# Optimization experiments

Measured on AMD Instinct MI355X. Metric: run time of the kernel, lower is better.

The kernel has to match this reference:

```python
import jax, jax.numpy as jnp
import numpy as np

B, N, F_IN, H = 16, 1024, 64, 256
NEG = -9e15
ALPHA = 0.2  # LeakyReLU slope


def _leaky(x):
    return jnp.where(x >= 0, x, ALPHA * x)


def setup_inputs() -> dict:
    key = jax.random.key(0)
    ks = jax.random.split(key, 12)
    s = lambda k, shape, fan: jax.random.normal(k, shape, jnp.float32) / np.sqrt(fan)
    node_features = jax.random.normal(ks[0], (B, N, F_IN), jnp.float32)
    adj_matrix = jax.random.randint(ks[1], (B, N, N), 0, 2).astype(jnp.float32)
    return {
        "node_features": node_features,
        "adj_matrix": adj_matrix,
        "emb_W": s(ks[2], (F_IN, H), F_IN),
        "emb_b": jnp.zeros((H,), jnp.float32),
        "W0": s(ks[3], (H, H), H),
        "a1_0": s(ks[4], (H,), H),
        "a2_0": s(ks[5], (H,), H),
        "W1": s(ks[6], (H, H), H),
        "a1_1": s(ks[7], (H,), H),
        "a2_1": s(ks[8], (H,), H),
        "gp_W1": s(ks[9], (H, H), H),
        "gp_b1": jnp.zeros((H,), jnp.float32),
        "gp_W2": s(ks[10], (H, H), H),
        "gp_b2": jnp.zeros((H,), jnp.float32),
    }


def _gat_layer(x, mask, W, a1, a2):
    # x: [B,N,H]; mask: [B,N,N] bool. Equivalent to original concat trick:
    # a([h_i || h_j]) = h_i @ a1 + h_j @ a2 with a.weight split in halves.
    h = jnp.einsum('bnf,fo->bno', x, W)              # [B,N,H]
    s1 = jnp.einsum('bnh,h->bn', h, a1)              # [B,N]
    s2 = jnp.einsum('bnh,h->bn', h, a2)              # [B,N]
    e = _leaky(s1[:, :, None] + s2[:, None, :])      # [B,N,N]
    att = jax.nn.softmax(jnp.where(mask, e, NEG), axis=2)
    # dropout p=0.2 is identity in eval mode
    return jnp.einsum('bij,bjh->bih', att, h)        # [B,N,H]


def reference(node_features, adj_matrix, emb_W, emb_b,
              W0, a1_0, a2_0, W1, a1_1, a2_1,
              gp_W1, gp_b1, gp_W2, gp_b2):
    mask = adj_matrix > 0
    x = jnp.einsum('bnf,fh->bnh', node_features, emb_W) + emb_b
    x = jax.nn.relu(_gat_layer(x, mask, W0, a1_0, a2_0))
    x = jax.nn.relu(_gat_layer(x, mask, W1, a1_1, a2_1))
    g = jnp.mean(x, axis=1) + jnp.max(x, axis=1)     # [B,H]
    g = jax.nn.relu(g @ gp_W1 + gp_b1) @ gp_W2 + gp_b2
    return x, g
```

## Files before the change

kernel.cpp:

```cpp
#include <hip/hip_runtime.h>
#include <hip/hip_bf16.h>

#define B 16
#define N 1024
#define F_IN 64
#define H 256
#define ALPHA 0.2f

typedef __attribute__((ext_vector_type(8))) _Float16 half8;
typedef __attribute__((ext_vector_type(4))) _Float16 half4;
typedef __attribute__((ext_vector_type(4))) float floatx4;

__device__ __forceinline__ floatx4 mfma_f16(half8 a, half8 b, floatx4 c) {
    return __builtin_amdgcn_mfma_f32_16x16x32_f16(a, b, c, 0, 0, 0);
}

__global__ __launch_bounds__(256) void k_front(const float* __restrict__ adj,
                                               const float* __restrict__ nf,
                                               const float* __restrict__ embW,
                                               const float* __restrict__ embB,
                                               const float* __restrict__ W0, const float* __restrict__ W1,
                                               const float* __restrict__ a10, const float* __restrict__ a20,
                                               const float* __restrict__ a11, const float* __restrict__ a21,
                                               unsigned* __restrict__ mask32,
                                               _Float16* __restrict__ xf,
                                               _Float16* __restrict__ wBf,
                                               float* __restrict__ wa1, float* __restrict__ wa2) {
    __shared__ float lds[256 * 17];
    const int blk = blockIdx.x;
    const int t = threadIdx.x;
    const int lane = t & 63;

    if (blk < 1024) {
        const int wv = blk * 4 + (t >> 6);
#pragma unroll 2
        for (int task = wv; task < B * N * 4; task += 4096) {
            const float4 v = *(const float4*)(adj + (size_t)task * 256 + lane * 4);
            unsigned long long b0 = __ballot(v.x > 0.f);
            unsigned long long b1 = __ballot(v.y > 0.f);
            unsigned long long b2 = __ballot(v.z > 0.f);
            unsigned long long b3 = __ballot(v.w > 0.f);
            if (lane < 8) {
                unsigned w0 = (unsigned)((b0 >> (8 * lane)) & 0xff)
                            | ((unsigned)((b1 >> (8 * lane)) & 0xff) << 8)
                            | ((unsigned)((b2 >> (8 * lane)) & 0xff) << 16)
                            | ((unsigned)((b3 >> (8 * lane)) & 0xff) << 24);
                const int jg = task & 3, row = task >> 2;
                mask32[(size_t)row * 32 + jg * 8 + lane] = w0;
            }
        }
        return;
    }
    if (blk < 1536) {
        const int row0 = (blk - 1024) * 32;
        float* nfs = lds;
        for (int idx = t; idx < 32 * F_IN; idx += 256) {
            int r = idx >> 6, f = idx & 63;
            nfs[f * 32 + r] = nf[(size_t)(row0 + r) * F_IN + f];
        }
        __syncthreads();
        const int c = t;
        float acc[32];
        const float bv = embB[c];
#pragma unroll
        for (int r = 0; r < 32; r++) acc[r] = bv;
#pragma unroll 8
        for (int f = 0; f < F_IN; f++) {
            const float w = embW[f * H + c];
            const float* nrow = nfs + f * 32;
#pragma unroll
            for (int q = 0; q < 8; q++) {
                float4 n4 = *(const float4*)(nrow + q * 4);
                acc[q * 4 + 0] += n4.x * w;
                acc[q * 4 + 1] += n4.y * w;
                acc[q * 4 + 2] += n4.z * w;
                acc[q * 4 + 3] += n4.w * w;
            }
        }
#pragma unroll
        for (int r = 0; r < 32; r++)
            xf[(size_t)(row0 + r) * H + c] = (_Float16)acc[r];
        return;
    }
    const int pb = blk - 1536;
    if (pb >= 32) {
        const int l = pb - 32;
        const float* W = l ? W1 : W0;
        const float* a1 = l ? a11 : a10;
        const float* a2 = l ? a21 : a20;
        float* a1s = lds;
        float* a2s = lds + 256;
        a1s[t] = a1[t]; a2s[t] = a2[t];
        __syncthreads();
        float v1 = 0.f, v2 = 0.f;
        for (int c = 0; c < H; c += 4) {
            float4 w = *(const float4*)&W[t * H + c];
            v1 += w.x * a1s[c] + w.y * a1s[c + 1] + w.z * a1s[c + 2] + w.w * a1s[c + 3];
            v2 += w.x * a2s[c] + w.y * a2s[c + 1] + w.z * a2s[c + 2] + w.w * a2s[c + 3];
        }
        wa1[l * H + t] = v1;
        wa2[l * H + t] = v2;
        return;
    }
    const int l = pb >> 4, ct = pb & 15;
    const float* W = l ? W1 : W0;
#pragma unroll
    for (int rep = 0; rep < 16; rep++) {
        int idx = rep * 256 + t;
        int k = idx >> 4, cl = idx & 15;
        lds[k * 17 + cl] = W[k * H + ct * 16 + cl];
    }
    __syncthreads();
    const int w = t >> 6;
    const int l15 = lane & 15, quad = lane >> 4;
#pragma unroll
    for (int e = 0; e < 2; e++) {
        const int ks = w * 2 + e;
        half8 bf;
#pragma unroll
        for (int jj = 0; jj < 8; jj++)
            bf[jj] = (_Float16)lds[(ks * 32 + quad * 8 + jj) * 17 + l15];
        *(half8*)(wBf + (size_t)(((l * 16 + ct) * 8 + ks) * 64 + lane) * 8) = bf;
    }
}

#define XS(it, ks) ((((it) * 8 + (ks))) * 520)
__global__ __launch_bounds__(256, 4) void k_gemm(const _Float16* __restrict__ xf,
                                                 const _Float16* __restrict__ wBf,
                                                 const float* __restrict__ wa1, const float* __restrict__ wa2,
                                                 _Float16* __restrict__ hB,
                                                 float* __restrict__ s1, float* __restrict__ s2) {
    __shared__ __align__(16) _Float16 sm[8320];
    const int lin = blockIdx.x;
    const int rc = lin >> 1, chalf = lin & 1;
    const int row0 = rc * 32;
    const int t = threadIdx.x;
    const int lane = t & 63, w = t >> 6;
    const int l15 = lane & 15, quad = lane >> 4;

#pragma unroll
    for (int pass = 0; pass < 4; pass++) {
        int idx = pass * 256 + t;
        int row_l = idx >> 5, k8 = idx & 31;
        half8 v = *(const half8*)(xf + (size_t)(row0 + row_l) * H + k8 * 8);
        int it = row_l >> 4, lf = row_l & 15, ks = k8 >> 2, qd = k8 & 3;
        *(half8*)(sm + XS(it, ks) + (qd * 16 + lf) * 8) = v;
    }
    __syncthreads();

    const int ct0 = chalf * 8 + 2 * w;
    const _Float16* pB0 = wBf + (size_t)((ct0 * 8) * 64 + lane) * 8;
    const _Float16* pB1 = wBf + (size_t)(((ct0 + 1) * 8) * 64 + lane) * 8;

    floatx4 acc[2][2];
    floatx4 z = {0.f, 0.f, 0.f, 0.f};
    acc[0][0] = z; acc[0][1] = z; acc[1][0] = z; acc[1][1] = z;
    float sp1a = 0.f, sp2a = 0.f, sp1b = 0.f, sp2b = 0.f;

    half8 B0 = *(const half8*)(pB0);
    half8 B1 = *(const half8*)(pB1);

#pragma unroll
    for (int ks = 0; ks < 8; ks++) {
        half8 nB0 = B0, nB1 = B1;
        if (ks < 7) {
            const int o = (ks + 1) * 512;
            nB0 = *(const half8*)(pB0 + o);
            nB1 = *(const half8*)(pB1 + o);
        }
        half8 A0 = *(const half8*)(sm + XS(0, ks) + lane * 8);
        half8 A1 = *(const half8*)(sm + XS(1, ks) + lane * 8);
        acc[0][0] = mfma_f16(A0, B0, acc[0][0]);
        acc[0][1] = mfma_f16(A0, B1, acc[0][1]);
        acc[1][0] = mfma_f16(A1, B0, acc[1][0]);
        acc[1][1] = mfma_f16(A1, B1, acc[1][1]);
        if (chalf == 0 && w == 0) {
            float4 w1a = *(const float4*)(wa1 + ks * 32 + quad * 8);
            float4 w1b = *(const float4*)(wa1 + ks * 32 + quad * 8 + 4);
            float4 w2a = *(const float4*)(wa2 + ks * 32 + quad * 8);
            float4 w2b = *(const float4*)(wa2 + ks * 32 + quad * 8 + 4);
            float wv1[8] = {w1a.x, w1a.y, w1a.z, w1a.w, w1b.x, w1b.y, w1b.z, w1b.w};
            float wv2[8] = {w2a.x, w2a.y, w2a.z, w2a.w, w2b.x, w2b.y, w2b.z, w2b.w};
#pragma unroll
            for (int j = 0; j < 8; j++) {
                float xa = (float)A0[j];
                float xb = (float)A1[j];
                sp1a += xa * wv1[j]; sp2a += xa * wv2[j];
                sp1b += xb * wv1[j]; sp2b += xb * wv2[j];
            }
        }
        B0 = nB0; B1 = nB1;
    }

    __syncthreads();
    _Float16* trc = sm;
#pragma unroll
    for (int rg = 0; rg < 2; rg++) {
#pragma unroll
        for (int n2 = 0; n2 < 2; n2++) {
            const int c_l = (2 * w + n2) * 16 + l15;
            half4 hv;
            hv[0] = (_Float16)acc[rg][n2][0];
            hv[1] = (_Float16)acc[rg][n2][1];
            hv[2] = (_Float16)acc[rg][n2][2];
            hv[3] = (_Float16)acc[rg][n2][3];
            *(half4*)(trc + c_l * 40 + rg * 16 + quad * 4) = hv;
        }
    }
    __syncthreads();
    {
        const int ct_l = t >> 5, sub = t & 31;
        const int bb = row0 >> 10, jt = (row0 >> 5) & 31;
        _Float16* dst = hB + (size_t)(((bb * 16 + chalf * 8 + ct_l) * 32 + jt) * 64) * 8;
#pragma unroll
        for (int rep = 0; rep < 2; rep++) {
            int lo = sub + rep * 32;
            int qd = lo >> 4, lf = lo & 15;
            half8 hv = *(const half8*)(trc + (ct_l * 16 + lf) * 40 + qd * 8);
            *(half8*)(dst + lo * 8) = hv;
        }
    }
    if (chalf == 0 && w == 0) {
        sp1a += __shfl_xor(sp1a, 16); sp1a += __shfl_xor(sp1a, 32);
        sp2a += __shfl_xor(sp2a, 16); sp2a += __shfl_xor(sp2a, 32);
        sp1b += __shfl_xor(sp1b, 16); sp1b += __shfl_xor(sp1b, 32);
        sp2b += __shfl_xor(sp2b, 16); sp2b += __shfl_xor(sp2b, 32);
        if (quad == 0) {
            s1[row0 + l15] = sp1a; s2[row0 + l15] = sp2a;
            s1[row0 + 16 + l15] = sp1b; s2[row0 + 16 + l15] = sp2b;
        }
    }
}

template <int LAST>
__global__ __launch_bounds__(256, 2) void k_gat(const _Float16* __restrict__ hB,
                                                const float* __restrict__ s1g,
                                                const float* __restrict__ s2g,
                                                const unsigned* __restrict__ mask32,
                                                float* __restrict__ outf,
                                                _Float16* __restrict__ oxf,
                                                float* __restrict__ psum, float* __restrict__ pmax) {
    __shared__ float s2s[N];
    __shared__ unsigned msk[64][33];
    __shared__ float wmax[4];
    __shared__ float l_s[64];
    __shared__ float red1[4][128];
    __shared__ float red2[4][128];
    const int lin = blockIdx.x;
    const int xcd = lin & 7, sl = lin >> 3;
    const int b = xcd * 2 + (sl & 1);
    const int chunk = (sl >> 1) & 15;
    const int chalf = sl >> 5;
    const int i0 = chunk * 64;
    const int t = threadIdx.x;
    const int lane = t & 63, w = t >> 6;
    const int l15 = lane & 15, quad = lane >> 4;
    const int ct0 = chalf * 8;

    float tm = -INFINITY;
    for (int idx = t; idx < N; idx += 256) {
        float v = s2g[b * N + idx];
        s2s[idx] = v;
        tm = fmaxf(tm, v);
    }
#pragma unroll
    for (int off = 1; off <= 32; off <<= 1) tm = fmaxf(tm, __shfl_xor(tm, off));
    if (lane == 0) wmax[w] = tm;
#pragma unroll
    for (int pass = 0; pass < 8; pass++) {
        int idx = pass * 256 + t;
        int r = idx >> 5, wd = idx & 31;
        msk[r][wd] = mask32[(size_t)(b * N + i0 + r) * 32 + wd];
    }
    __syncthreads();
    const float s2max = fmaxf(fmaxf(wmax[0], wmax[1]), fmaxf(wmax[2], wmax[3]));

    const float s1v = s1g[b * N + i0 + w * 16 + l15];
    const float tmx = s1v + s2max;
    const float mrow = fmaxf(tmx, ALPHA * tmx);

    const _Float16* pb[8];
#pragma unroll
    for (int k = 0; k < 8; k++)
        pb[k] = hB + (size_t)((b * 16 + ct0 + k) * 32 * 64) * 8 + lane * 8;

    floatx4 acc[8];
    floatx4 z = {0.f, 0.f, 0.f, 0.f};
#pragma unroll
    for (int k = 0; k < 8; k++) acc[k] = z;
    float lacc = 0.f;

    half8 cB[8];
#pragma unroll
    for (int k = 0; k < 8; k++) cB[k] = *(const half8*)(pb[k]);

    for (int jt = 0; jt < 32; jt++) {
        half8 nB[8];
        if (jt < 31) {
            const int o = (jt + 1) * 512;
#pragma unroll
            for (int k = 0; k < 8; k++) nB[k] = *(const half8*)(pb[k] + o);
        }
        unsigned mwq = msk[w * 16 + l15][jt] >> (quad * 2);
        float4 sa = *(const float4*)&s2s[jt * 32 + quad * 8];
        float4 sb = *(const float4*)&s2s[jt * 32 + quad * 8 + 4];
        float sv[8] = {sa.x, sa.y, sa.z, sa.w, sb.x, sb.y, sb.z, sb.w};
        union { _Float16 h[8]; half8 v; } pk;
#pragma unroll
        for (int jj = 0; jj < 8; jj++) {
            float e = s1v + sv[jj];
            e = fmaxf(e, ALPHA * e);
            float p = __expf(e - mrow);
            p = ((mwq >> ((jj & 3) * 8 + (jj >> 2))) & 1u) ? p : 0.f;
            pk.h[jj] = (_Float16)p;
            lacc += (float)pk.h[jj];
        }
        half8 A = pk.v;
#pragma unroll
        for (int k = 0; k < 8; k++) acc[k] = mfma_f16(A, cB[k], acc[k]);
        if (jt < 31) {
#pragma unroll
            for (int k = 0; k < 8; k++) cB[k] = nB[k];
        }
    }

    lacc += __shfl_xor(lacc, 16);
    lacc += __shfl_xor(lacc, 32);
    if (quad == 0) l_s[w * 16 + l15] = lacc;
    __syncthreads();

    float inv[4];
#pragma unroll
    for (int r = 0; r < 4; r++) inv[r] = 1.f / l_s[w * 16 + quad * 4 + r];

    const size_t rbase = (size_t)b * N + i0 + w * 16 + quad * 4;
#pragma unroll
    for (int k = 0; k < 8; k++) {
        const int c = (ct0 + k) * 16 + l15;
        float cs = 0.f, cm = -INFINITY;
#pragma unroll
        for (int r = 0; r < 4; r++) {
            float v = fmaxf(acc[k][r] * inv[r], 0.f);
            if (LAST) {
                outf[(rbase + r) * H + c] = v;
                cs += v; cm = fmaxf(cm, v);
            } else {
                oxf[(rbase + r) * H + c] = (_Float16)v;
            }
        }
        if (LAST) {
            cs += __shfl_xor(cs, 16); cs += __shfl_xor(cs, 32);
            cm = fmaxf(cm, __shfl_xor(cm, 16)); cm = fmaxf(cm, __shfl_xor(cm, 32));
            if (quad == 0) { red1[w][k * 16 + l15] = cs; red2[w][k * 16 + l15] = cm; }
        }
    }
    if (LAST) {
        __syncthreads();
        if (t < 128) {
            float s = red1[0][t] + red1[1][t] + red1[2][t] + red1[3][t];
            float m = fmaxf(fmaxf(red2[0][t], red2[1][t]), fmaxf(red2[2][t], red2[3][t]));
            psum[(b * 16 + chunk) * H + chalf * 128 + t] = s;
            pmax[(b * 16 + chunk) * H + chalf * 128 + t] = m;
        }
    }
}

__global__ __launch_bounds__(256) void k_pool2(const float* __restrict__ psum,
                                               const float* __restrict__ pmax,
                                               const float* __restrict__ W1, const float* __restrict__ b1,
                                               const float* __restrict__ W2, const float* __restrict__ b2,
                                               float* __restrict__ gout) {
    __shared__ float g_s[H];
    __shared__ float t_s[H];
    const int b = blockIdx.x;
    const int c = threadIdx.x;
    float s = 0.f, m = -INFINITY;
#pragma unroll
    for (int ch = 0; ch < 16; ch++) {
        s += psum[(b * 16 + ch) * H + c];
        m = fmaxf(m, pmax[(b * 16 + ch) * H + c]);
    }
    g_s[c] = s * (1.f / N) + m;
    __syncthreads();
    float a = b1[c];
#pragma unroll 16
    for (int k = 0; k < H; k++) a += g_s[k] * W1[k * H + c];
    t_s[c] = fmaxf(a, 0.f);
    __syncthreads();
    float o = b2[c];
#pragma unroll 16
    for (int k = 0; k < H; k++) o += t_s[k] * W2[k * H + c];
    gout[b * H + c] = o;
}

extern "C" void kernel_launch(void* const* d_in, const int* in_sizes, int n_in,
                              void* d_out, int out_size, void* d_ws, size_t ws_size,
                              hipStream_t stream) {
    const float* nf    = (const float*)d_in[0];
    const float* adj   = (const float*)d_in[1];
    const float* emb_W = (const float*)d_in[2];
    const float* emb_b = (const float*)d_in[3];
    const float* W0    = (const float*)d_in[4];
    const float* a1_0  = (const float*)d_in[5];
    const float* a2_0  = (const float*)d_in[6];
    const float* W1    = (const float*)d_in[7];
    const float* a1_1  = (const float*)d_in[8];
    const float* a2_1  = (const float*)d_in[9];
    const float* gpW1  = (const float*)d_in[10];
    const float* gpb1  = (const float*)d_in[11];
    const float* gpW2  = (const float*)d_in[12];
    const float* gpb2  = (const float*)d_in[13];

    float* xout = (float*)d_out;
    float* gout = xout + B * N * H;

    char* w = (char*)d_ws;
    _Float16* xf     = (_Float16*)(w);
    _Float16* hB     = (_Float16*)(w + 8388608);
    unsigned* mask32 = (unsigned*)(w + 16777216);
    float* s1        = (float*)(w + 18874368);
    float* s2        = (float*)(w + 18939904);
    _Float16* wBf    = (_Float16*)(w + 19005440);
    float* wa1       = (float*)(w + 19267584);
    float* wa2       = (float*)(w + 19269632);
    float* psum      = (float*)(w + 19271680);
    float* pmax      = (float*)(w + 19533824);

    k_front<<<1570, 256, 0, stream>>>(adj, nf, emb_W, emb_b, W0, W1,
                                      a1_0, a2_0, a1_1, a2_1,
                                      mask32, xf, wBf, wa1, wa2);

    k_gemm<<<1024, 256, 0, stream>>>(xf, wBf, wa1, wa2, hB, s1, s2);
    k_gat<0><<<512, 256, 0, stream>>>(hB, s1, s2, mask32, nullptr, xf,
                                      nullptr, nullptr);

    k_gemm<<<1024, 256, 0, stream>>>(xf, wBf + 65536, wa1 + H, wa2 + H, hB, s1, s2);
    k_gat<1><<<512, 256, 0, stream>>>(hB, s1, s2, mask32, xout, nullptr,
                                      psum, pmax);

    k_pool2<<<B, 256, 0, stream>>>(psum, pmax, gpW1, gpb1, gpW2, gpb2, gout);
}
```

Measured before the change: 225.2 us.

## Retile GAT attention waves to 32 rows x 64 cols and use exp2 softmax

Each wave now handles 32 query rows and 4 column tiles instead of 16 rows and 8 column tiles. This halves the per-wave B-operand (h) global loads, which are reused across two A fragments, and double-buffers them with explicit ping-pong. The softmax now works in log2 space, prescaling s1/s2 by log2(e) and folding the leaky max into two fmas, and uses the hardware exp2. Masked entries go through exp2(-126) instead of a zero select, and the row sum now adds the fp32 probabilities rather than the fp16-rounded ones. This is a slight numerical difference, and the exp work per wave is doubled because each wave now covers twice the rows.

```diff
diff --git a/kernel.cpp b/kernel.cpp
--- a/kernel.cpp
+++ b/kernel.cpp
@@ -6,10 +6,17 @@
 #define F_IN 64
 #define H 256
 #define ALPHA 0.2f
+#define LOG2E 1.44269504f
 
 typedef __attribute__((ext_vector_type(8))) _Float16 half8;
 typedef __attribute__((ext_vector_type(4))) _Float16 half4;
 typedef __attribute__((ext_vector_type(4))) float floatx4;
+
+#if __has_builtin(__builtin_amdgcn_exp2f)
+#define EXP2F(x) __builtin_amdgcn_exp2f(x)
+#else
+#define EXP2F(x) exp2f(x)
+#endif
 
 __device__ __forceinline__ floatx4 mfma_f16(half8 a, half8 b, floatx4 c) {
     return __builtin_amdgcn_mfma_f32_16x16x32_f16(a, b, c, 0, 0, 0);
@@ -244,8 +251,8 @@
     __shared__ unsigned msk[64][33];
     __shared__ float wmax[4];
     __shared__ float l_s[64];
-    __shared__ float red1[4][128];
-    __shared__ float red2[4][128];
+    __shared__ float red1[2][128];
+    __shared__ float red2[2][128];
     const int lin = blockIdx.x;
     const int xcd = lin & 7, sl = lin >> 3;
     const int b = xcd * 2 + (sl & 1);
@@ -255,11 +262,12 @@
     const int t = threadIdx.x;
     const int lane = t & 63, w = t >> 6;
     const int l15 = lane & 15, quad = lane >> 4;
-    const int ct0 = chalf * 8;
+    const int wi = w & 1, wc = w >> 1;
+    const int ct0 = chalf * 8 + wc * 4;
 
     float tm = -INFINITY;
     for (int idx = t; idx < N; idx += 256) {
-        float v = s2g[b * N + idx];
+        float v = s2g[b * N + idx] * LOG2E;
         s2s[idx] = v;
         tm = fmaxf(tm, v);
     }
@@ -273,92 +281,133 @@
         msk[r][wd] = mask32[(size_t)(b * N + i0 + r) * 32 + wd];
     }
     __syncthreads();
-    const float s2max = fmaxf(fmaxf(wmax[0], wmax[1]), fmaxf(wmax[2], wmax[3]));
-
-    const float s1v = s1g[b * N + i0 + w * 16 + l15];
-    const float tmx = s1v + s2max;
-    const float mrow = fmaxf(tmx, ALPHA * tmx);
-
-    const _Float16* pb[8];
-#pragma unroll
-    for (int k = 0; k < 8; k++)
+    const float s2maxL = fmaxf(fmaxf(wmax[0], wmax[1]), fmaxf(wmax[2], wmax[3]));
+
+    float a1c[2], a2c[2];
+#pragma unroll
+    for (int it2 = 0; it2 < 2; it2++) {
+        float s1L = s1g[b * N + i0 + wi * 32 + it2 * 16 + l15] * LOG2E;
+        float tmx = s1L + s2maxL;
+        float mL = fmaxf(tmx, ALPHA * tmx);
+        a1c[it2] = s1L - mL;
+        a2c[it2] = fmaf(ALPHA, s1L, -mL);
+    }
+
+    const _Float16* pb[4];
+#pragma unroll
+    for (int k = 0; k < 4; k++)
         pb[k] = hB + (size_t)((b * 16 + ct0 + k) * 32 * 64) * 8 + lane * 8;
 
-    floatx4 acc[8];
+    floatx4 acc[2][4];
     floatx4 z = {0.f, 0.f, 0.f, 0.f};
 #pragma unroll
-    for (int k = 0; k < 8; k++) acc[k] = z;
-    float lacc = 0.f;
-
-    half8 cB[8];
-#pragma unroll
-    for (int k = 0; k < 8; k++) cB[k] = *(const half8*)(pb[k]);
-
-    for (int jt = 0; jt < 32; jt++) {
-        half8 nB[8];
-        if (jt < 31) {
+    for (int it2 = 0; it2 < 2; it2++)
+#pragma unroll
+        for (int k = 0; k < 4; k++) acc[it2][k] = z;
+    float lacc0 = 0.f, lacc1 = 0.f;
+
+    const float* svp = s2s + quad * 8;
+    const unsigned* mr0 = &msk[wi * 32 + l15][0];
+    const unsigned* mr1 = &msk[wi * 32 + 16 + l15][0];
+
+    half8 bufA[4], bufB[4];
+#pragma unroll
+    for (int k = 0; k < 4; k++) bufA[k] = *(const half8*)(pb[k]);
+
+#define GAT_STEP(JT, BUF)                                                      \
+    do {                                                                       \
+        float4 sa = *(const float4*)(svp + (JT) * 32);                         \
+        float4 sb = *(const float4*)(svp + (JT) * 32 + 4);                     \
+        float sv[8] = {sa.x, sa.y, sa.z, sa.w, sb.x, sb.y, sb.z, sb.w};        \
+        unsigned mq0 = mr0[JT] >> (quad * 2);                                  \
+        unsigned mq1 = mr1[JT] >> (quad * 2);                                  \
+        union { _Float16 h[8]; half8 v; } pk0, pk1;                            \
+        _Pragma("unroll")                                                      \
+        for (int jj = 0; jj < 8; jj++) {                                       \
+            const int bp = (jj & 3) * 8 + (jj >> 2);                           \
+            float u0 = a1c[0] + sv[jj];                                        \
+            float v0 = fmaf(ALPHA, sv[jj], a2c[0]);                            \
+            float w0 = fmaxf(u0, v0);                                          \
+            w0 = ((mq0 >> bp) & 1u) ? w0 : -126.f;                             \
+            float p0 = EXP2F(w0);                                              \
+            lacc0 += p0;                                                       \
+            pk0.h[jj] = (_Float16)p0;                                          \
+            float u1 = a1c[1] + sv[jj];                                        \
+            float v1 = fmaf(ALPHA, sv[jj], a2c[1]);                            \
+            float w1 = fmaxf(u1, v1);                                          \
+            w1 = ((mq1 >> bp) & 1u) ? w1 : -126.f;                             \
+            float p1 = EXP2F(w1);                                              \
+            lacc1 += p1;                                                       \
+            pk1.h[jj] = (_Float16)p1;                                          \
+        }                                                                      \
+        _Pragma("unroll")                                                      \
+        for (int k = 0; k < 4; k++) acc[0][k] = mfma_f16(pk0.v, BUF[k], acc[0][k]); \
+        _Pragma("unroll")                                                      \
+        for (int k = 0; k < 4; k++) acc[1][k] = mfma_f16(pk1.v, BUF[k], acc[1][k]); \
+    } while (0)
+
+    for (int jt = 0; jt < 32; jt += 2) {
+        {
             const int o = (jt + 1) * 512;
 #pragma unroll
-            for (int k = 0; k < 8; k++) nB[k] = *(const half8*)(pb[k] + o);
-        }
-        unsigned mwq = msk[w * 16 + l15][jt] >> (quad * 2);
-        float4 sa = *(const float4*)&s2s[jt * 32 + quad * 8];
-        float4 sb = *(const float4*)&s2s[jt * 32 + quad * 8 + 4];
-        float sv[8] = {sa.x, sa.y, sa.z, sa.w, sb.x, sb.y, sb.z, sb.w};
-        union { _Float16 h[8]; half8 v; } pk;
-#pragma unroll
-        for (int jj = 0; jj < 8; jj++) {
-            float e = s1v + sv[jj];
-            e = fmaxf(e, ALPHA * e);
-            float p = __expf(e - mrow);
-            p = ((mwq >> ((jj & 3) * 8 + (jj >> 2))) & 1u) ? p : 0.f;
-            pk.h[jj] = (_Float16)p;
-            lacc += (float)pk.h[jj];
-        }
-        half8 A = pk.v;
-#pragma unroll
-        for (int k = 0; k < 8; k++) acc[k] = mfma_f16(A, cB[k], acc[k]);
-        if (jt < 31) {
-#pragma unroll
-            for (int k = 0; k < 8; k++) cB[k] = nB[k];
-        }
-    }
-
-    lacc += __shfl_xor(lacc, 16);
-    lacc += __shfl_xor(lacc, 32);
-    if (quad == 0) l_s[w * 16 + l15] = lacc;
-    __syncthreads();
-
-    float inv[4];
-#pragma unroll
-    for (int r = 0; r < 4; r++) inv[r] = 1.f / l_s[w * 16 + quad * 4 + r];
-
-    const size_t rbase = (size_t)b * N + i0 + w * 16 + quad * 4;
-#pragma unroll
-    for (int k = 0; k < 8; k++) {
+            for (int k = 0; k < 4; k++) bufB[k] = *(const half8*)(pb[k] + o);
+        }
+        GAT_STEP(jt, bufA);
+        if (jt + 2 < 32) {
+            const int o = (jt + 2) * 512;
+#pragma unroll
+            for (int k = 0; k < 4; k++) bufA[k] = *(const half8*)(pb[k] + o);
+        }
+        GAT_STEP(jt + 1, bufB);
+    }
+#undef GAT_STEP
+
+    lacc0 += __shfl_xor(lacc0, 16); lacc0 += __shfl_xor(lacc0, 32);
+    lacc1 += __shfl_xor(lacc1, 16); lacc1 += __shfl_xor(lacc1, 32);
+    if (wc == 0 && quad == 0) {
+        l_s[wi * 32 + l15] = lacc0;
+        l_s[wi * 32 + 16 + l15] = lacc1;
+    }
+    __syncthreads();
+
+    float inv[2][4];
+#pragma unroll
+    for (int it2 = 0; it2 < 2; it2++)
+#pragma unroll
+        for (int r = 0; r < 4; r++)
+            inv[it2][r] = 1.f / l_s[wi * 32 + it2 * 16 + quad * 4 + r];
+
+    const size_t rbase = (size_t)b * N + i0 + wi * 32 + quad * 4;
+#pragma unroll
+    for (int k = 0; k < 4; k++) {
         const int c = (ct0 + k) * 16 + l15;
         float cs = 0.f, cm = -INFINITY;
 #pragma unroll
-        for (int r = 0; r < 4; r++) {
-            float v = fmaxf(acc[k][r] * inv[r], 0.f);
-            if (LAST) {
-                outf[(rbase + r) * H + c] = v;
-                cs += v; cm = fmaxf(cm, v);
-            } else {
-                oxf[(rbase + r) * H + c] = (_Float16)v;
+        for (int it2 = 0; it2 < 2; it2++)
+#pragma unroll
+            for (int r = 0; r < 4; r++) {
+                float v = fmaxf(acc[it2][k][r] * inv[it2][r], 0.f);
+                if (LAST) {
+                    outf[(rbase + it2 * 16 + r) * H + c] = v;
+                    cs += v; cm = fmaxf(cm, v);
+                } else {
+                    oxf[(rbase + it2 * 16 + r) * H + c] = (_Float16)v;
+                }
             }
-        }
         if (LAST) {
             cs += __shfl_xor(cs, 16); cs += __shfl_xor(cs, 32);
             cm = fmaxf(cm, __shfl_xor(cm, 16)); cm = fmaxf(cm, __shfl_xor(cm, 32));
-            if (quad == 0) { red1[w][k * 16 + l15] = cs; red2[w][k * 16 + l15] = cm; }
+            if (quad == 0) {
+                red1[wi][(wc * 4 + k) * 16 + l15] = cs;
+                red2[wi][(wc * 4 + k) * 16 + l15] = cm;
+            }
         }
     }
     if (LAST) {
         __syncthreads();
         if (t < 128) {
-            float s = red1[0][t] + red1[1][t] + red1[2][t] + red1[3][t];
-            float m = fmaxf(fmaxf(red2[0][t], red2[1][t]), fmaxf(red2[2][t], red2[3][t]));
+            float s = red1[0][t] + red1[1][t];
+            float m = fmaxf(red2[0][t], red2[1][t]);
             psum[(b * 16 + chunk) * H + chalf * 128 + t] = s;
             pmax[(b * 16 + chunk) * H + chalf * 128 + t] = m;
         }
```

Measured after the change: 231.1 us. +2.7%, slower.

## Use exp2 with prescaled scores, MFMA row sums, and ping-pong B buffers

Applied to the files above, without the earlier changes.

Scales s1/s2 by log2(e) up front so the LeakyReLU-exponent becomes a max of two affine terms fed to a native exp2. Masked entries now go to exp2(-126) instead of a select to zero. The softmax denominator is accumulated with an extra MFMA against a ones vector, which replaces the per-lane scalar adds, the shuffles and the LDS barrier. The loop is unrolled by two with double-buffered B loads so register copies between iterations go away. Masked entries now add a tiny nonzero weight, and register pressure rises.

```diff
diff --git a/kernel.cpp b/kernel.cpp
--- a/kernel.cpp
+++ b/kernel.cpp
@@ -6,10 +6,17 @@
 #define F_IN 64
 #define H 256
 #define ALPHA 0.2f
+#define LOG2E 1.44269504f
 
 typedef __attribute__((ext_vector_type(8))) _Float16 half8;
 typedef __attribute__((ext_vector_type(4))) _Float16 half4;
 typedef __attribute__((ext_vector_type(4))) float floatx4;
+
+#if __has_builtin(__builtin_amdgcn_exp2f)
+#define EXP2F(x) __builtin_amdgcn_exp2f(x)
+#else
+#define EXP2F(x) exp2f(x)
+#endif
 
 __device__ __forceinline__ floatx4 mfma_f16(half8 a, half8 b, floatx4 c) {
     return __builtin_amdgcn_mfma_f32_16x16x32_f16(a, b, c, 0, 0, 0);
@@ -243,7 +250,6 @@
     __shared__ float s2s[N];
     __shared__ unsigned msk[64][33];
     __shared__ float wmax[4];
-    __shared__ float l_s[64];
     __shared__ float red1[4][128];
     __shared__ float red2[4][128];
     const int lin = blockIdx.x;
@@ -259,7 +265,7 @@
 
     float tm = -INFINITY;
     for (int idx = t; idx < N; idx += 256) {
-        float v = s2g[b * N + idx];
+        float v = s2g[b * N + idx] * LOG2E;
         s2s[idx] = v;
         tm = fmaxf(tm, v);
     }
@@ -273,11 +279,13 @@
         msk[r][wd] = mask32[(size_t)(b * N + i0 + r) * 32 + wd];
     }
     __syncthreads();
-    const float s2max = fmaxf(fmaxf(wmax[0], wmax[1]), fmaxf(wmax[2], wmax[3]));
-
-    const float s1v = s1g[b * N + i0 + w * 16 + l15];
-    const float tmx = s1v + s2max;
-    const float mrow = fmaxf(tmx, ALPHA * tmx);
+    const float s2maxL = fmaxf(fmaxf(wmax[0], wmax[1]), fmaxf(wmax[2], wmax[3]));
+
+    const float s1L = s1g[b * N + i0 + w * 16 + l15] * LOG2E;
+    const float tmx = s1L + s2maxL;
+    const float mL = fmaxf(tmx, ALPHA * tmx);
+    const float a1c = s1L - mL;
+    const float a2c = fmaf(ALPHA, s1L, -mL);
 
     const _Float16* pb[8];
 #pragma unroll
@@ -288,50 +296,59 @@
     floatx4 z = {0.f, 0.f, 0.f, 0.f};
 #pragma unroll
     for (int k = 0; k < 8; k++) acc[k] = z;
-    float lacc = 0.f;
-
-    half8 cB[8];
-#pragma unroll
-    for (int k = 0; k < 8; k++) cB[k] = *(const half8*)(pb[k]);
-
-    for (int jt = 0; jt < 32; jt++) {
-        half8 nB[8];
-        if (jt < 31) {
+    floatx4 accl = z;
+
+    half8 ones;
+#pragma unroll
+    for (int jj = 0; jj < 8; jj++) ones[jj] = (_Float16)1.0f;
+
+    const float* svp = s2s + quad * 8;
+    const unsigned* mr = &msk[w * 16 + l15][0];
+
+    half8 bufA[8], bufB[8];
+#pragma unroll
+    for (int k = 0; k < 8; k++) bufA[k] = *(const half8*)(pb[k]);
+
+#define GAT_STEP(JT, BUF)                                                      \
+    do {                                                                       \
+        float4 sa = *(const float4*)(svp + (JT) * 32);                         \
+        float4 sb = *(const float4*)(svp + (JT) * 32 + 4);                     \
+        float sv[8] = {sa.x, sa.y, sa.z, sa.w, sb.x, sb.y, sb.z, sb.w};        \
+        unsigned mq = mr[JT] >> (quad * 2);                                    \
+        union { _Float16 h[8]; half8 v; } pk;                                  \
+        _Pragma("unroll")                                                      \
+        for (int jj = 0; jj < 8; jj++) {                                       \
+            const int bp = (jj & 3) * 8 + (jj >> 2);                           \
+            float u = a1c + sv[jj];                                            \
+            float v2 = fmaf(ALPHA, sv[jj], a2c);                               \
+            float e = fmaxf(u, v2);                                            \
+            e = ((mq >> bp) & 1u) ? e : -126.f;                                \
+            pk.h[jj] = (_Float16)EXP2F(e);                                     \
+        }                                                                      \
+        accl = mfma_f16(pk.v, ones, accl);                                     \
+        _Pragma("unroll")                                                      \
+        for (int k = 0; k < 8; k++) acc[k] = mfma_f16(pk.v, BUF[k], acc[k]);   \
+    } while (0)
+
+    for (int jt = 0; jt < 32; jt += 2) {
+        {
             const int o = (jt + 1) * 512;
 #pragma unroll
-            for (int k = 0; k < 8; k++) nB[k] = *(const half8*)(pb[k] + o);
-        }
-        unsigned mwq = msk[w * 16 + l15][jt] >> (quad * 2);
-        float4 sa = *(const float4*)&s2s[jt * 32 + quad * 8];
-        float4 sb = *(const float4*)&s2s[jt * 32 + quad * 8 + 4];
-        float sv[8] = {sa.x, sa.y, sa.z, sa.w, sb.x, sb.y, sb.z, sb.w};
-        union { _Float16 h[8]; half8 v; } pk;
-#pragma unroll
-        for (int jj = 0; jj < 8; jj++) {
-            float e = s1v + sv[jj];
-            e = fmaxf(e, ALPHA * e);
-            float p = __expf(e - mrow);
-            p = ((mwq >> ((jj & 3) * 8 + (jj >> 2))) & 1u) ? p : 0.f;
-            pk.h[jj] = (_Float16)p;
-            lacc += (float)pk.h[jj];
-        }
-        half8 A = pk.v;
-#pragma unroll
-        for (int k = 0; k < 8; k++) acc[k] = mfma_f16(A, cB[k], acc[k]);
-        if (jt < 31) {
-#pragma unroll
-            for (int k = 0; k < 8; k++) cB[k] = nB[k];
-        }
-    }
-
-    lacc += __shfl_xor(lacc, 16);
-    lacc += __shfl_xor(lacc, 32);
-    if (quad == 0) l_s[w * 16 + l15] = lacc;
-    __syncthreads();
+            for (int k = 0; k < 8; k++) bufB[k] = *(const half8*)(pb[k] + o);
+        }
+        GAT_STEP(jt, bufA);
+        if (jt + 2 < 32) {
+            const int o = (jt + 2) * 512;
+#pragma unroll
+            for (int k = 0; k < 8; k++) bufA[k] = *(const half8*)(pb[k] + o);
+        }
+        GAT_STEP(jt + 1, bufB);
+    }
+#undef GAT_STEP
 
     float inv[4];
 #pragma unroll
-    for (int r = 0; r < 4; r++) inv[r] = 1.f / l_s[w * 16 + quad * 4 + r];
+    for (int r = 0; r < 4; r++) inv[r] = 1.f / accl[r];
 
     const size_t rbase = (size_t)b * N + i0 + w * 16 + quad * 4;
 #pragma unroll
```

New measurement: 221.2 us. About the same (-1.8%).
